# Kernel tuning notes

Hardware: AMD Instinct MI355X
Metric: run time of the kernel (lower is better)

## Reference

```python
import jax, jax.numpy as jnp
import numpy as np

EPS = 1e-5
NEG_SLOPE = 0.01  # nn.LeakyReLU default


def _bn(x, gamma, beta, mean, var):
    # eval-mode batchnorm over last (channel) axis
    return (x - mean) * (gamma * jax.lax.rsqrt(var + EPS)) + beta


def setup_inputs() -> dict:
    key = jax.random.key(0)
    ks = jax.random.split(key, 12)
    B, N, F = 4, 256, 128
    Cin = 2 * F + 2  # edge channels (2) + pairwise concat (2F)
    inp = {
        "node_feat": jax.random.normal(ks[0], (B, N, F), jnp.float32),
        "edge_feat": jax.random.normal(ks[1], (B, N, N, 2), jnp.float32),
        # conv1: 1x1, (2F+2) -> F, no bias
        "w1": jax.random.normal(ks[2], (F, Cin), jnp.float32) * (1.0 / np.sqrt(Cin)),
        "bn1_gamma": jnp.ones((F,), jnp.float32),
        "bn1_beta": jnp.zeros((F,), jnp.float32),
        "bn1_mean": jnp.zeros((F,), jnp.float32),
        "bn1_var": jnp.ones((F,), jnp.float32),
        # conv2: 1x1, F -> F, no bias
        "w2": jax.random.normal(ks[3], (F, F), jnp.float32) * (1.0 / np.sqrt(F)),
        "bn2_gamma": jnp.ones((F,), jnp.float32),
        "bn2_beta": jnp.zeros((F,), jnp.float32),
        "bn2_mean": jnp.zeros((F,), jnp.float32),
        "bn2_var": jnp.ones((F,), jnp.float32),
        # pair_network: Linear(F, 2)
        "pw": jax.random.normal(ks[4], (2, F), jnp.float32) * (1.0 / np.sqrt(F)),
        "pb": jax.random.uniform(ks[5], (2,), jnp.float32, -0.1, 0.1),
    }
    return inp


def reference(node_feat, edge_feat, w1, bn1_gamma, bn1_beta, bn1_mean, bn1_var,
              w2, bn2_gamma, bn2_beta, bn2_mean, bn2_var, pw, pb):
    # node_feat: [B,N,F], edge_feat: [B,N,N,2]
    F = node_feat.shape[-1]
    # concat order along channels: [edge (2), P_left (F), P_right (F)]
    w_e = w1[:, :2]            # [F, 2]
    w_l = w1[:, 2:2 + F]       # [F, F]
    w_r = w1[:, 2 + F:]        # [F, F]
    # Fused broadcast-GEMM: conv1x1 over concat == sum of partial projections.
    hl = jnp.einsum('bif,gf->big', node_feat, w_l)   # [B,N,F] (row/left term)
    hr = jnp.einsum('bjf,gf->bjg', node_feat, w_r)   # [B,N,F] (col/right term)
    he = jnp.einsum('bijc,gc->bijg', edge_feat, w_e)  # [B,N,N,F]
    h = he + hl[:, :, None, :] + hr[:, None, :, :]    # [B,N,N,F]
    h = _bn(h, bn1_gamma, bn1_beta, bn1_mean, bn1_var)
    h = jnp.where(h >= 0, h, NEG_SLOPE * h)           # LeakyReLU
    # Dropout is identity in eval mode.
    h = jnp.einsum('bijf,gf->bijg', h, w2)            # conv2 1x1
    h = _bn(h, bn2_gamma, bn2_beta, bn2_mean, bn2_var)
    out = jnp.einsum('bijf,of->bijo', h, pw) + pb     # [B,N,N,2]
    return out
```

## Files before the change

kernel.cpp:

```cpp
#include <hip/hip_runtime.h>

#define EPS    1e-5f
#define NSLOPE 0.01f
#define B 4
#define N 256
#define F 128

#define WS_WE0 0
#define WS_WE1 128
#define WS_PF0 256
#define WS_PF1 384
#define WS_C   512
#define WS_HL  1024
#define WS_HR  (WS_HL + B*N*F)

__global__ __launch_bounds__(128) void prep_all(
    const float* __restrict__ node, const float* __restrict__ w1,
    const float* __restrict__ g1, const float* __restrict__ b1,
    const float* __restrict__ m1, const float* __restrict__ v1,
    const float* __restrict__ w2, const float* __restrict__ g2,
    const float* __restrict__ b2, const float* __restrict__ m2,
    const float* __restrict__ v2, const float* __restrict__ pw,
    const float* __restrict__ pb, float* __restrict__ ws) {
  if (blockIdx.x == 256) {
    __shared__ float s2s[F], t2s[F];
    int g = threadIdx.x;
    float s1v = g1[g] / sqrtf(v1[g] + EPS);
    ws[WS_WE0 + g] = w1[g * 258 + 0] * s1v;
    ws[WS_WE1 + g] = w1[g * 258 + 1] * s1v;
    float s2v = g2[g] / sqrtf(v2[g] + EPS);
    s2s[g] = s2v;
    t2s[g] = b2[g] - m2[g] * s2v;
    __syncthreads();
    float a0 = 0.f, a1 = 0.f;
    for (int f = 0; f < F; ++f) {
      float wv = w2[f * F + g];
      a0 = fmaf(pw[f]     * s2s[f], wv, a0);
      a1 = fmaf(pw[F + f] * s2s[f], wv, a1);
    }
    ws[WS_PF0 + g] = a0;
    ws[WS_PF1 + g] = a1;
    if (g < 2) {
      float c = pb[g];
      for (int f = 0; f < F; ++f) c += pw[g * F + f] * t2s[f];
      ws[WS_C + g] = c;
    }
    return;
  }
  __shared__ float4 ns4[64 * 32];
  __shared__ float  wlds[2][8][F];
  int t = threadIdx.x;
  int rc = blockIdx.x >> 4;
  int gc = blockIdx.x & 15;
  int r0 = rc * 64;
  int gb = gc * 8;
  const float4* node4 = reinterpret_cast<const float4*>(node) + (size_t)r0 * 32;
  #pragma unroll
  for (int k = 0; k < 16; ++k) {
    int L = k * 128 + t;
    int row = L >> 5, s = L & 31;
    ns4[row * 32 + (s ^ (row & 7))] = node4[L];
  }
  #pragma unroll
  for (int k = 0; k < 8; ++k) {
    const float* wrow = w1 + (size_t)(gb + k) * 258;
    wlds[0][k][t] = wrow[2 + t];
    wlds[1][k][t] = wrow[130 + t];
  }
  __syncthreads();
  int lane = t & 63;
  int wv = __builtin_amdgcn_readfirstlane(t >> 6);
  int lx = lane & 7;
  int lbase = lane * 32;
  float accl[4] = {0.f, 0.f, 0.f, 0.f};
  float accr[4] = {0.f, 0.f, 0.f, 0.f};
  #pragma unroll 4
  for (int q = 0; q < 32; ++q) {
    float4 nv = ns4[lbase + (q ^ lx)];
    #pragma unroll
    for (int k = 0; k < 4; ++k) {
      int kk = wv * 4 + k;
      float4 wl = *reinterpret_cast<const float4*>(&wlds[0][kk][q * 4]);
      float4 wr = *reinterpret_cast<const float4*>(&wlds[1][kk][q * 4]);
      accl[k] = fmaf(nv.x, wl.x, accl[k]);
      accl[k] = fmaf(nv.y, wl.y, accl[k]);
      accl[k] = fmaf(nv.z, wl.z, accl[k]);
      accl[k] = fmaf(nv.w, wl.w, accl[k]);
      accr[k] = fmaf(nv.x, wr.x, accr[k]);
      accr[k] = fmaf(nv.y, wr.y, accr[k]);
      accr[k] = fmaf(nv.z, wr.z, accr[k]);
      accr[k] = fmaf(nv.w, wr.w, accr[k]);
    }
  }
  int row = r0 + lane;
  int g0 = gb + wv * 4;
  float4 ol, orr;
  #pragma unroll
  for (int k = 0; k < 4; ++k) {
    int g = g0 + k;
    float s1v = g1[g] / sqrtf(v1[g] + EPS);
    float t1v = b1[g] - m1[g] * s1v;
    (&ol.x)[k]  = fmaf(accl[k], s1v, t1v);
    (&orr.x)[k] = accr[k] * s1v;
  }
  *reinterpret_cast<float4*>(ws + WS_HL + (size_t)row * F + g0) = ol;
  *reinterpret_cast<float4*>(ws + WS_HR + (size_t)row * F + g0) = orr;
}

__global__ __launch_bounds__(512) void fused_main(
    const float* __restrict__ edge,
    const float* __restrict__ ws, float* __restrict__ out) {
  __shared__ float hls[32][132];
  __shared__ float hrs[32][132];
  int b = blockIdx.z, i0 = blockIdx.y * 32, j0 = blockIdx.x * 32;
  int t = threadIdx.x;
  int ti = t >> 4, tj = t & 15;
  int i1 = i0 + ti, j1 = j0 + tj, j2 = j1 + 16;
  float2 e0 = *reinterpret_cast<const float2*>(edge + ((size_t)(b * N + i1) * N + j1) * 2);
  float2 e1 = *reinterpret_cast<const float2*>(edge + ((size_t)(b * N + i1) * N + j2) * 2);
  {
    int r = t >> 4, c0 = (t & 15) * 8;
    const float* sl = ws + WS_HL + (size_t)(b * N + i0 + r) * F + c0;
    const float* sr = ws + WS_HR + (size_t)(b * N + j0 + r) * F + c0;
    *reinterpret_cast<float4*>(&hls[r][c0])     = *reinterpret_cast<const float4*>(sl);
    *reinterpret_cast<float4*>(&hls[r][c0 + 4]) = *reinterpret_cast<const float4*>(sl + 4);
    *reinterpret_cast<float4*>(&hrs[r][c0])     = *reinterpret_cast<const float4*>(sr);
    *reinterpret_cast<float4*>(&hrs[r][c0 + 4]) = *reinterpret_cast<const float4*>(sr + 4);
  }
  __syncthreads();
  const float4* W0p = reinterpret_cast<const float4*>(ws + WS_WE0);
  const float4* W1p = reinterpret_cast<const float4*>(ws + WS_WE1);
  const float4* P0p = reinterpret_cast<const float4*>(ws + WS_PF0);
  const float4* P1p = reinterpret_cast<const float4*>(ws + WS_PF1);
  float a0x = 0.f, a0y = 0.f, a1x = 0.f, a1y = 0.f;
  #pragma unroll 4
  for (int gq = 0; gq < F / 4; ++gq) {
    int g = gq * 4;
    float4 L  = *reinterpret_cast<const float4*>(&hls[ti][g]);
    float4 R0 = *reinterpret_cast<const float4*>(&hrs[tj][g]);
    float4 R1 = *reinterpret_cast<const float4*>(&hrs[tj + 16][g]);
    float4 W0 = W0p[gq];
    float4 W1 = W1p[gq];
    float4 P0 = P0p[gq];
    float4 P1 = P1p[gq];
#define DO_COMP(K)                                                             \
    {                                                                          \
      float w0 = W0.K, w1v = W1.K, p0 = P0.K, p1 = P1.K;                       \
      float v;                                                                 \
      v = L.K + R0.K; v = fmaf(e0.x, w0, v); v = fmaf(e0.y, w1v, v);           \
      v = fmaxf(v, NSLOPE * v);                                                \
      a0x = fmaf(p0, v, a0x); a0y = fmaf(p1, v, a0y);                          \
      v = L.K + R1.K; v = fmaf(e1.x, w0, v); v = fmaf(e1.y, w1v, v);           \
      v = fmaxf(v, NSLOPE * v);                                                \
      a1x = fmaf(p0, v, a1x); a1y = fmaf(p1, v, a1y);                          \
    }
    DO_COMP(x) DO_COMP(y) DO_COMP(z) DO_COMP(w)
#undef DO_COMP
  }
  float c0 = ws[WS_C + 0], c1 = ws[WS_C + 1];
  float2 o;
  o.x = a0x + c0; o.y = a0y + c1;
  *reinterpret_cast<float2*>(out + ((size_t)(b * N + i1) * N + j1) * 2) = o;
  o.x = a1x + c0; o.y = a1y + c1;
  *reinterpret_cast<float2*>(out + ((size_t)(b * N + i1) * N + j2) * 2) = o;
}

extern "C" void kernel_launch(void* const* d_in, const int* in_sizes, int n_in,
                              void* d_out, int out_size, void* d_ws, size_t ws_size,
                              hipStream_t stream) {
  const float* node = (const float*)d_in[0];
  const float* edge = (const float*)d_in[1];
  const float* w1   = (const float*)d_in[2];
  const float* g1   = (const float*)d_in[3];
  const float* b1   = (const float*)d_in[4];
  const float* m1   = (const float*)d_in[5];
  const float* v1   = (const float*)d_in[6];
  const float* w2   = (const float*)d_in[7];
  const float* g2   = (const float*)d_in[8];
  const float* b2   = (const float*)d_in[9];
  const float* m2   = (const float*)d_in[10];
  const float* v2   = (const float*)d_in[11];
  const float* pw   = (const float*)d_in[12];
  const float* pb   = (const float*)d_in[13];
  float* ws  = (float*)d_ws;
  float* out = (float*)d_out;

  prep_all<<<257, 128, 0, stream>>>(node, w1, g1, b1, m1, v1, w2, g2, b2, m2,
                                    v2, pw, pb, ws);
  fused_main<<<dim3(N / 32, N / 32, B), 512, 0, stream>>>(edge, ws, out);
}
```

Measured before the change: 25.61 us.

## Merge prep and main kernels into one cooperative kernel with grid sync

Combines the projection/prep kernel and the fused pairwise kernel into a single cooperative launch of 256 blocks. The first phase computes the hl/hr projections and folded constants using 128 threads per block, then a grid-wide barrier replaces the kernel boundary before the main pairwise phase. Edge loads are issued before the barrier so they overlap the prep phase. The intent is to remove the second launch and its gap. In exchange it adds grid-sync overhead, leaves most threads idle during prep, and relies on all 256 blocks being co-resident.

```diff
diff --git a/kernel.cpp b/kernel.cpp
--- a/kernel.cpp
+++ b/kernel.cpp
@@ -1,4 +1,7 @@
 #include <hip/hip_runtime.h>
+#include <hip/hip_cooperative_groups.h>
+
+namespace cg = cooperative_groups;
 
 #define EPS    1e-5f
 #define NSLOPE 0.01f
@@ -14,29 +17,98 @@
 #define WS_HL  1024
 #define WS_HR  (WS_HL + B*N*F)
 
-__global__ __launch_bounds__(128) void prep_all(
-    const float* __restrict__ node, const float* __restrict__ w1,
-    const float* __restrict__ g1, const float* __restrict__ b1,
-    const float* __restrict__ m1, const float* __restrict__ v1,
-    const float* __restrict__ w2, const float* __restrict__ g2,
-    const float* __restrict__ b2, const float* __restrict__ m2,
-    const float* __restrict__ v2, const float* __restrict__ pw,
-    const float* __restrict__ pb, float* __restrict__ ws) {
-  if (blockIdx.x == 256) {
-    __shared__ float s2s[F], t2s[F];
-    int g = threadIdx.x;
+__global__ __launch_bounds__(512, 2) void fused_coop(
+    const float* __restrict__ node, const float* __restrict__ edge,
+    const float* __restrict__ w1, const float* __restrict__ g1,
+    const float* __restrict__ b1, const float* __restrict__ m1,
+    const float* __restrict__ v1, const float* __restrict__ w2,
+    const float* __restrict__ g2, const float* __restrict__ b2,
+    const float* __restrict__ m2, const float* __restrict__ v2,
+    const float* __restrict__ pw, const float* __restrict__ pb,
+    float* ws, float* __restrict__ out) {
+  __shared__ __align__(16) char smem[40960];
+  __shared__ float s2s[F], t2s[F];
+  int t = threadIdx.x;
+  int b = blockIdx.z, i0 = blockIdx.y * 32, j0 = blockIdx.x * 32;
+  int bid = (b * 8 + (int)blockIdx.y) * 8 + (int)blockIdx.x;
+  int ti = t >> 4, tj = t & 15;
+  int i1 = i0 + ti, j1 = j0 + tj, j2 = j1 + 16;
+  float2 e0 = *reinterpret_cast<const float2*>(edge + ((size_t)(b * N + i1) * N + j1) * 2);
+  float2 e1 = *reinterpret_cast<const float2*>(edge + ((size_t)(b * N + i1) * N + j2) * 2);
+
+  float4* ns4 = reinterpret_cast<float4*>(smem);
+  float (*wlds)[8][F] = reinterpret_cast<float(*)[8][F]>(smem + 32768);
+  int rc = bid >> 4, gc = bid & 15;
+  int r0p = rc * 64, gb = gc * 8;
+  if (t < 128) {
+    const float4* node4 = reinterpret_cast<const float4*>(node) + (size_t)r0p * 32;
+    #pragma unroll
+    for (int k = 0; k < 16; ++k) {
+      int L = k * 128 + t;
+      int row = L >> 5, s = L & 31;
+      ns4[row * 32 + (s ^ (row & 7))] = node4[L];
+    }
+    #pragma unroll
+    for (int k = 0; k < 8; ++k) {
+      const float* wrow = w1 + (size_t)(gb + k) * 258;
+      wlds[0][k][t] = wrow[2 + t];
+      wlds[1][k][t] = wrow[130 + t];
+    }
+  } else if (bid == 0 && t < 256) {
+    int g = t - 128;
     float s1v = g1[g] / sqrtf(v1[g] + EPS);
     ws[WS_WE0 + g] = w1[g * 258 + 0] * s1v;
     ws[WS_WE1 + g] = w1[g * 258 + 1] * s1v;
     float s2v = g2[g] / sqrtf(v2[g] + EPS);
     s2s[g] = s2v;
     t2s[g] = b2[g] - m2[g] * s2v;
-    __syncthreads();
+  }
+  __syncthreads();
+  if (t < 128) {
+    int lane = t & 63;
+    int wv = __builtin_amdgcn_readfirstlane(t >> 6);
+    int lx = lane & 7;
+    int lbase = lane * 32;
+    float accl[4] = {0.f, 0.f, 0.f, 0.f};
+    float accr[4] = {0.f, 0.f, 0.f, 0.f};
+    #pragma unroll 4
+    for (int q = 0; q < 32; ++q) {
+      float4 nv = ns4[lbase + (q ^ lx)];
+      #pragma unroll
+      for (int k = 0; k < 4; ++k) {
+        int kk = wv * 4 + k;
+        float4 wl = *reinterpret_cast<const float4*>(&wlds[0][kk][q * 4]);
+        float4 wr = *reinterpret_cast<const float4*>(&wlds[1][kk][q * 4]);
+        accl[k] = fmaf(nv.x, wl.x, accl[k]);
+        accl[k] = fmaf(nv.y, wl.y, accl[k]);
+        accl[k] = fmaf(nv.z, wl.z, accl[k]);
+        accl[k] = fmaf(nv.w, wl.w, accl[k]);
+        accr[k] = fmaf(nv.x, wr.x, accr[k]);
+        accr[k] = fmaf(nv.y, wr.y, accr[k]);
+        accr[k] = fmaf(nv.z, wr.z, accr[k]);
+        accr[k] = fmaf(nv.w, wr.w, accr[k]);
+      }
+    }
+    int row = r0p + lane;
+    int g0 = gb + wv * 4;
+    float4 ol, orr;
+    #pragma unroll
+    for (int k = 0; k < 4; ++k) {
+      int g = g0 + k;
+      float s1v = g1[g] / sqrtf(v1[g] + EPS);
+      float t1v = b1[g] - m1[g] * s1v;
+      (&ol.x)[k]  = fmaf(accl[k], s1v, t1v);
+      (&orr.x)[k] = accr[k] * s1v;
+    }
+    *reinterpret_cast<float4*>(ws + WS_HL + (size_t)row * F + g0) = ol;
+    *reinterpret_cast<float4*>(ws + WS_HR + (size_t)row * F + g0) = orr;
+  } else if (bid == 0 && t < 256) {
+    int g = t - 128;
     float a0 = 0.f, a1 = 0.f;
     for (int f = 0; f < F; ++f) {
-      float wv = w2[f * F + g];
-      a0 = fmaf(pw[f]     * s2s[f], wv, a0);
-      a1 = fmaf(pw[F + f] * s2s[f], wv, a1);
+      float wv2 = w2[f * F + g];
+      a0 = fmaf(pw[f]     * s2s[f], wv2, a0);
+      a1 = fmaf(pw[F + f] * s2s[f], wv2, a1);
     }
     ws[WS_PF0 + g] = a0;
     ws[WS_PF1 + g] = a1;
@@ -45,79 +117,12 @@
       for (int f = 0; f < F; ++f) c += pw[g * F + f] * t2s[f];
       ws[WS_C + g] = c;
     }
-    return;
-  }
-  __shared__ float4 ns4[64 * 32];
-  __shared__ float  wlds[2][8][F];
-  int t = threadIdx.x;
-  int rc = blockIdx.x >> 4;
-  int gc = blockIdx.x & 15;
-  int r0 = rc * 64;
-  int gb = gc * 8;
-  const float4* node4 = reinterpret_cast<const float4*>(node) + (size_t)r0 * 32;
-  #pragma unroll
-  for (int k = 0; k < 16; ++k) {
-    int L = k * 128 + t;
-    int row = L >> 5, s = L & 31;
-    ns4[row * 32 + (s ^ (row & 7))] = node4[L];
-  }
-  #pragma unroll
-  for (int k = 0; k < 8; ++k) {
-    const float* wrow = w1 + (size_t)(gb + k) * 258;
-    wlds[0][k][t] = wrow[2 + t];
-    wlds[1][k][t] = wrow[130 + t];
-  }
-  __syncthreads();
-  int lane = t & 63;
-  int wv = __builtin_amdgcn_readfirstlane(t >> 6);
-  int lx = lane & 7;
-  int lbase = lane * 32;
-  float accl[4] = {0.f, 0.f, 0.f, 0.f};
-  float accr[4] = {0.f, 0.f, 0.f, 0.f};
-  #pragma unroll 4
-  for (int q = 0; q < 32; ++q) {
-    float4 nv = ns4[lbase + (q ^ lx)];
-    #pragma unroll
-    for (int k = 0; k < 4; ++k) {
-      int kk = wv * 4 + k;
-      float4 wl = *reinterpret_cast<const float4*>(&wlds[0][kk][q * 4]);
-      float4 wr = *reinterpret_cast<const float4*>(&wlds[1][kk][q * 4]);
-      accl[k] = fmaf(nv.x, wl.x, accl[k]);
-      accl[k] = fmaf(nv.y, wl.y, accl[k]);
-      accl[k] = fmaf(nv.z, wl.z, accl[k]);
-      accl[k] = fmaf(nv.w, wl.w, accl[k]);
-      accr[k] = fmaf(nv.x, wr.x, accr[k]);
-      accr[k] = fmaf(nv.y, wr.y, accr[k]);
-      accr[k] = fmaf(nv.z, wr.z, accr[k]);
-      accr[k] = fmaf(nv.w, wr.w, accr[k]);
-    }
-  }
-  int row = r0 + lane;
-  int g0 = gb + wv * 4;
-  float4 ol, orr;
-  #pragma unroll
-  for (int k = 0; k < 4; ++k) {
-    int g = g0 + k;
-    float s1v = g1[g] / sqrtf(v1[g] + EPS);
-    float t1v = b1[g] - m1[g] * s1v;
-    (&ol.x)[k]  = fmaf(accl[k], s1v, t1v);
-    (&orr.x)[k] = accr[k] * s1v;
-  }
-  *reinterpret_cast<float4*>(ws + WS_HL + (size_t)row * F + g0) = ol;
-  *reinterpret_cast<float4*>(ws + WS_HR + (size_t)row * F + g0) = orr;
-}
-
-__global__ __launch_bounds__(512) void fused_main(
-    const float* __restrict__ edge,
-    const float* __restrict__ ws, float* __restrict__ out) {
-  __shared__ float hls[32][132];
-  __shared__ float hrs[32][132];
-  int b = blockIdx.z, i0 = blockIdx.y * 32, j0 = blockIdx.x * 32;
-  int t = threadIdx.x;
-  int ti = t >> 4, tj = t & 15;
-  int i1 = i0 + ti, j1 = j0 + tj, j2 = j1 + 16;
-  float2 e0 = *reinterpret_cast<const float2*>(edge + ((size_t)(b * N + i1) * N + j1) * 2);
-  float2 e1 = *reinterpret_cast<const float2*>(edge + ((size_t)(b * N + i1) * N + j2) * 2);
+  }
+
+  cg::this_grid().sync();
+
+  float (*hls)[132] = reinterpret_cast<float(*)[132]>(smem);
+  float (*hrs)[132] = reinterpret_cast<float(*)[132]>(smem + 32 * 132 * 4);
   {
     int r = t >> 4, c0 = (t & 15) * 8;
     const float* sl = ws + WS_HL + (size_t)(b * N + i0 + r) * F + c0;
@@ -157,11 +162,11 @@
     DO_COMP(x) DO_COMP(y) DO_COMP(z) DO_COMP(w)
 #undef DO_COMP
   }
-  float c0 = ws[WS_C + 0], c1 = ws[WS_C + 1];
+  float c0v = ws[WS_C + 0], c1v = ws[WS_C + 1];
   float2 o;
-  o.x = a0x + c0; o.y = a0y + c1;
+  o.x = a0x + c0v; o.y = a0y + c1v;
   *reinterpret_cast<float2*>(out + ((size_t)(b * N + i1) * N + j1) * 2) = o;
-  o.x = a1x + c0; o.y = a1y + c1;
+  o.x = a1x + c0v; o.y = a1y + c1v;
   *reinterpret_cast<float2*>(out + ((size_t)(b * N + i1) * N + j2) * 2) = o;
 }
 
@@ -185,7 +190,11 @@
   float* ws  = (float*)d_ws;
   float* out = (float*)d_out;
 
-  prep_all<<<257, 128, 0, stream>>>(node, w1, g1, b1, m1, v1, w2, g2, b2, m2,
-                                    v2, pw, pb, ws);
-  fused_main<<<dim3(N / 32, N / 32, B), 512, 0, stream>>>(edge, ws, out);
+  void* args[16] = {
+      (void*)&node, (void*)&edge, (void*)&w1, (void*)&g1, (void*)&b1,
+      (void*)&m1,   (void*)&v1,   (void*)&w2, (void*)&g2, (void*)&b2,
+      (void*)&m2,   (void*)&v2,   (void*)&pw, (void*)&pb, (void*)&ws,
+      (void*)&out};
+  hipLaunchCooperativeKernel((const void*)fused_coop, dim3(N / 32, N / 32, B),
+                             dim3(512), args, 0, stream);
 }
```

Measured after the change: 73.45 us. 2.87x slower.
